# Kernel tuning notes

Hardware: AMD Instinct MI355X
Metric: run time of the kernel (lower is better)

Reference implementation:

```python
import jax, jax.numpy as jnp
import numpy as np

N_NODES = 100000
N_EDGES = 1600000
D_IN, D_HID, N_CLASSES = 128, 128, 64


def setup_inputs() -> dict:
    key = jax.random.key(0)
    k1, k2, k3, k4 = jax.random.split(key, 4)
    x = jax.random.normal(k1, (N_NODES, D_IN), dtype=jnp.float32)
    edge_index = jax.random.randint(k2, (2, N_EDGES), 0, N_NODES, dtype=jnp.int64)
    W1 = jax.random.normal(k3, (D_IN, D_HID), dtype=jnp.float32) * 0.05
    b1 = jnp.zeros((D_HID,), dtype=jnp.float32)
    W2 = jax.random.normal(k4, (D_HID, N_CLASSES), dtype=jnp.float32) * 0.05
    b2 = jnp.zeros((N_CLASSES,), dtype=jnp.float32)
    return {"x": x, "edge_index": edge_index, "W1": W1, "b1": b1, "W2": W2, "b2": b2}


def _gcn_layer(x, src_all, dst_all, edge_w, W, b):
    # PyG GCNConv: x' = D^{-1/2} (A + I) D^{-1/2} (x W) + b
    n = x.shape[0]
    h = x @ W                                   # [N, out]
    msg = h[src_all] * edge_w[:, None]          # [E+N, out]
    out = jax.ops.segment_sum(msg, dst_all, num_segments=n)
    return out + b


def reference(x, edge_index, W1, b1, W2, b2):
    n = x.shape[0]
    src, dst = edge_index[0], edge_index[1]
    loop = jnp.arange(n, dtype=src.dtype)
    src_all = jnp.concatenate([src, loop])      # self-loops added (GCNConv default)
    dst_all = jnp.concatenate([dst, loop])
    deg = jax.ops.segment_sum(jnp.ones_like(dst_all, dtype=x.dtype), dst_all,
                              num_segments=n)
    dinv = jnp.where(deg > 0, jax.lax.rsqrt(deg), 0.0)
    edge_w = dinv[src_all] * dinv[dst_all]      # symmetric normalization

    h = _gcn_layer(x, src_all, dst_all, edge_w, W1, b1)
    h = jax.nn.relu(h)                          # dropout is identity in eval mode
    h = _gcn_layer(h, src_all, dst_all, edge_w, W2, b2)
    return jax.nn.log_softmax(h, axis=1)
```

## Files before the change

### kernel.cpp

```cpp
#include <hip/hip_runtime.h>
#include <math.h>

#define DIN 128
#define NCLS 64
#define BSH  7
#define BSZ  128
#define BCAP 2816
#define SCALE1 64.0f
#define SCALE2 256.0f

typedef __attribute__((ext_vector_type(4))) float  f32x4;
typedef __attribute__((ext_vector_type(2))) float  f32x2;
typedef __attribute__((ext_vector_type(8))) short  bf16x8;

__device__ inline unsigned short f2bf(float f) {
    unsigned int u = __float_as_uint(f);
    u += 0x7fff + ((u >> 16) & 1);
    return (unsigned short)(u >> 16);
}


__global__ __launch_bounds__(256) void binA_k(const int* __restrict__ ei,
                                              int* __restrict__ gcnt,
                                              unsigned int* __restrict__ tmp,
                                              int E, int NB) {
    __shared__ int lcnt[1024];
    __shared__ int gpos[1024];
    const int t = threadIdx.x;
    for (int i = t; i < NB; i += 256) lcnt[i] = 0;
    __syncthreads();

    const int base = blockIdx.x * 4096;
    unsigned int pk[16];
    short bk[16], rk[16];
#pragma unroll
    for (int k = 0; k < 16; ++k) {
        int e = base + k * 256 + t;
        if (e < E) {
            int s = ei[e];
            int d = ei[E + e];
            int b = d >> BSH;
            pk[k] = ((unsigned int)s << BSH) | (unsigned int)(d & (BSZ - 1));
            bk[k] = (short)b;
            rk[k] = (short)atomicAdd(&lcnt[b], 1);
        } else {
            bk[k] = -1;
        }
    }
    __syncthreads();
    for (int i = t; i < NB; i += 256)
        gpos[i] = lcnt[i] ? atomicAdd(&gcnt[i], lcnt[i]) : 0;
    __syncthreads();
#pragma unroll
    for (int k = 0; k < 16; ++k) {
        if (bk[k] >= 0) {
            int b = bk[k];
            int pos = gpos[b] + rk[k];
            if (pos < BCAP) tmp[(size_t)b * BCAP + pos] = pk[k];
        }
    }
}

__global__ __launch_bounds__(1024) void scanb_k(const int* __restrict__ gcnt,
                                                int* __restrict__ bbase, int NB) {
    __shared__ int tmp[1024];
    int t = threadIdx.x;
    int v = (t < NB) ? gcnt[t] : 0;
    tmp[t] = v; __syncthreads();
    for (int o = 1; o < 1024; o <<= 1) {
        int x = (t >= o) ? tmp[t - o] : 0;
        __syncthreads();
        tmp[t] += x;
        __syncthreads();
    }
    if (t < NB) bbase[t] = (t == 0) ? 0 : tmp[t - 1];
}

__global__ __launch_bounds__(256) void binB_k(const unsigned int* __restrict__ tmp,
                                              const int* __restrict__ gcnt,
                                              const int* __restrict__ bbase,
                                              int* __restrict__ off,
                                              float* __restrict__ dinv,
                                              int* __restrict__ srcs,
                                              int N, int E) {
    __shared__ unsigned int stg[BCAP];
    __shared__ int lcnt[BSZ], sc[BSZ], loff[BSZ], lcur[BSZ];
    const int b = blockIdx.x, t = threadIdx.x;
    int cnt = gcnt[b];
    if (cnt > BCAP) cnt = BCAP;
    const int base = bbase[b];
    if (t < BSZ) { lcnt[t] = 0; lcur[t] = 0; }
    __syncthreads();
    for (int i = t; i < cnt; i += 256) {
        unsigned int v = tmp[(size_t)b * BCAP + i];
        stg[i] = v;
        atomicAdd(&lcnt[v & (BSZ - 1u)], 1);
    }
    __syncthreads();
    if (t < BSZ) sc[t] = lcnt[t];
    __syncthreads();
    for (int o = 1; o < BSZ; o <<= 1) {
        int x = 0;
        if (t < BSZ && t >= o) x = sc[t - o];
        __syncthreads();
        if (t < BSZ) sc[t] += x;
        __syncthreads();
    }
    if (t < BSZ) {
        int excl = (t == 0) ? 0 : sc[t - 1];
        loff[t] = excl;
        int node = b * BSZ + t;
        if (node <= N) off[node] = base + excl;
        if (node < N)  dinv[node] = rsqrtf(1.0f + (float)lcnt[t]);
    }
    __syncthreads();
    for (int i = t; i < cnt; i += 256) {
        unsigned int v = stg[i];
        int l = v & (BSZ - 1u);
        int r = atomicAdd(&lcur[l], 1);
        srcs[base + loff[l] + r] = (int)(v >> BSH);
    }
}


__global__ void wprep_k(const float* __restrict__ W1, const float* __restrict__ W2,
                        unsigned short* __restrict__ wt1, unsigned short* __restrict__ wt2,
                        int* __restrict__ gcnt, int NB) {
    int i = blockIdx.x * 256 + threadIdx.x;
    if (i < 128 * 128) { int k = i >> 7, n = i & 127; wt1[n * 128 + k] = f2bf(W1[i]); }
    if (i < 128 * 64)  { int k = i >> 6, n = i & 63;  wt2[n * 128 + k] = f2bf(W2[i]); }
    if (i < NB)        gcnt[i] = 0;
}


__global__ __launch_bounds__(256) void mgemm_k(const float* __restrict__ A,
                                               const unsigned short* __restrict__ Bt,
                                               const float* __restrict__ dinv,
                                               unsigned char* __restrict__ C,
                                               float oscale, int N) {
    constexpr int LDK = DIN + 8;
    constexpr int BN  = 128;
    __shared__ unsigned short As[64 * LDK];
    __shared__ unsigned short Bs[BN * LDK];
    const int tid  = threadIdx.x;
    const int row0 = blockIdx.x * 64;

    for (int idx = tid; idx < BN * 16; idx += 256) {
        int n = idx >> 4, c = (idx & 15) << 3;
        *(uint4*)&Bs[n * LDK + c] = *(const uint4*)&Bt[n * DIN + c];
    }
    for (int idx = tid; idx < 64 * 16; idx += 256) {
        int r = idx >> 4, c = (idx & 15) << 3;
        int gr = row0 + r;
        unsigned short v[8];
        if (gr < N) {
            f32x4 a0 = *(const f32x4*)&A[(size_t)gr * DIN + c];
            f32x4 a1 = *(const f32x4*)&A[(size_t)gr * DIN + c + 4];
            v[0] = f2bf(a0.x); v[1] = f2bf(a0.y); v[2] = f2bf(a0.z); v[3] = f2bf(a0.w);
            v[4] = f2bf(a1.x); v[5] = f2bf(a1.y); v[6] = f2bf(a1.z); v[7] = f2bf(a1.w);
        } else {
#pragma unroll
            for (int j = 0; j < 8; ++j) v[j] = 0;
        }
        *(uint4*)&As[r * LDK + c] = *(const uint4*)v;
    }
    __syncthreads();

    const int wave = tid >> 6, lane = tid & 63;
    const int lrow = lane & 15, kq = lane >> 4;
    constexpr int NT = BN / 16;
    f32x4 acc[NT];
#pragma unroll
    for (int t = 0; t < NT; ++t) acc[t] = (f32x4){0.f, 0.f, 0.f, 0.f};

    const unsigned short* Abase = &As[(wave * 16 + lrow) * LDK + kq * 8];
    const unsigned short* Bbase = &Bs[lrow * LDK + kq * 8];
#pragma unroll
    for (int kk = 0; kk < 4; ++kk) {
        bf16x8 a = *(const bf16x8*)(Abase + kk * 32);
#pragma unroll
        for (int t = 0; t < NT; ++t) {
            bf16x8 b = *(const bf16x8*)(Bbase + t * 16 * LDK + kk * 32);
            acc[t] = __builtin_amdgcn_mfma_f32_16x16x32_bf16(a, b, acc[t], 0, 0, 0);
        }
    }

    const int rb = row0 + wave * 16 + kq * 4;
#pragma unroll
    for (int r = 0; r < 4; ++r) {
        int gr = rb + r;
        if (gr < N) {
            float sc2 = dinv[gr] * oscale;
#pragma unroll
            for (int t = 0; t < NT; t += 2) {
                int pk = __builtin_amdgcn_cvt_pk_fp8_f32(acc[t][r] * sc2,
                                                         acc[t + 1][r] * sc2, 0, false);
                C[(size_t)gr * BN + t * 16 + lrow]       = (unsigned char)(pk & 0xff);
                C[(size_t)gr * BN + (t + 1) * 16 + lrow] = (unsigned char)((pk >> 8) & 0xff);
            }
        }
    }
}

__device__ inline void dec8(uint2 v, f32x2& x0, f32x2& x1, f32x2& x2, f32x2& x3) {
    x0 += __builtin_amdgcn_cvt_pk_f32_fp8((int)v.x, false);
    x1 += __builtin_amdgcn_cvt_pk_f32_fp8((int)v.x, true);
    x2 += __builtin_amdgcn_cvt_pk_f32_fp8((int)v.y, false);
    x3 += __builtin_amdgcn_cvt_pk_f32_fp8((int)v.y, true);
}

__device__ inline void dec16(uint4 v, f32x2& x0, f32x2& x1, f32x2& x2, f32x2& x3,
                             f32x2& x4, f32x2& x5, f32x2& x6, f32x2& x7) {
    x0 += __builtin_amdgcn_cvt_pk_f32_fp8((int)v.x, false);
    x1 += __builtin_amdgcn_cvt_pk_f32_fp8((int)v.x, true);
    x2 += __builtin_amdgcn_cvt_pk_f32_fp8((int)v.y, false);
    x3 += __builtin_amdgcn_cvt_pk_f32_fp8((int)v.y, true);
    x4 += __builtin_amdgcn_cvt_pk_f32_fp8((int)v.z, false);
    x5 += __builtin_amdgcn_cvt_pk_f32_fp8((int)v.z, true);
    x6 += __builtin_amdgcn_cvt_pk_f32_fp8((int)v.w, false);
    x7 += __builtin_amdgcn_cvt_pk_f32_fp8((int)v.w, true);
}


__global__ __launch_bounds__(512, 8) void fuse2_k(const unsigned char* __restrict__ hs,
                                                  const int* __restrict__ off,
                                                  const int* __restrict__ srcs,
                                                  const float* __restrict__ dinv,
                                                  const float* __restrict__ b1,
                                                  const unsigned short* __restrict__ Bt,
                                                  unsigned char* __restrict__ C,
                                                  int N) {
    constexpr int LDK = DIN + 8;
    __shared__ unsigned short As[64 * LDK];
    __shared__ unsigned short Bs[NCLS * LDK];
    const int tid  = threadIdx.x;
    const int row0 = blockIdx.x * 64;

    for (int idx = tid; idx < NCLS * 16; idx += 512) {
        int n = idx >> 4, c = (idx & 15) << 3;
        *(uint4*)&Bs[n * LDK + c] = *(const uint4*)&Bt[n * DIN + c];
    }

    const int oc = tid >> 3;
    const int sl = tid & 7;
    const int node = row0 + oc;
    const uint4* hp = (const uint4*)hs;

    if (node < N) {
        const int beg = off[node], end = off[node + 1];
        f32x2 a0={0.f,0.f},a1={0.f,0.f},a2={0.f,0.f},a3={0.f,0.f};
        f32x2 a4={0.f,0.f},a5={0.f,0.f},a6={0.f,0.f},a7={0.f,0.f};
        int i = beg;
        for (; i + 3 < end; i += 4) {
            unsigned s0 = (unsigned)srcs[i],     s1 = (unsigned)srcs[i + 1];
            unsigned s2 = (unsigned)srcs[i + 2], s3 = (unsigned)srcs[i + 3];
            uint4 v0 = hp[s0 * 8u + sl];
            uint4 v1 = hp[s1 * 8u + sl];
            uint4 v2 = hp[s2 * 8u + sl];
            uint4 v3 = hp[s3 * 8u + sl];
            dec16(v0, a0,a1,a2,a3,a4,a5,a6,a7);
            dec16(v1, a0,a1,a2,a3,a4,a5,a6,a7);
            dec16(v2, a0,a1,a2,a3,a4,a5,a6,a7);
            dec16(v3, a0,a1,a2,a3,a4,a5,a6,a7);
        }
        for (; i < end; ++i) {
            uint4 v = hp[(unsigned)srcs[i] * 8u + sl];
            dec16(v, a0,a1,a2,a3,a4,a5,a6,a7);
        }
        {
            uint4 v = hp[(unsigned)node * 8u + sl];
            dec16(v, a0,a1,a2,a3,a4,a5,a6,a7);
        }
        const float d = dinv[node] * (1.0f / SCALE1);
        const float4 w0 = ((const float4*)b1)[sl * 4 + 0];
        const float4 w1 = ((const float4*)b1)[sl * 4 + 1];
        const float4 w2 = ((const float4*)b1)[sl * 4 + 2];
        const float4 w3 = ((const float4*)b1)[sl * 4 + 3];
        float o0  = fmaxf(fmaf(d, a0.x, w0.x), 0.f);
        float o1  = fmaxf(fmaf(d, a0.y, w0.y), 0.f);
        float o2  = fmaxf(fmaf(d, a1.x, w0.z), 0.f);
        float o3  = fmaxf(fmaf(d, a1.y, w0.w), 0.f);
        float o4  = fmaxf(fmaf(d, a2.x, w1.x), 0.f);
        float o5  = fmaxf(fmaf(d, a2.y, w1.y), 0.f);
        float o6  = fmaxf(fmaf(d, a3.x, w1.z), 0.f);
        float o7  = fmaxf(fmaf(d, a3.y, w1.w), 0.f);
        float o8  = fmaxf(fmaf(d, a4.x, w2.x), 0.f);
        float o9  = fmaxf(fmaf(d, a4.y, w2.y), 0.f);
        float o10 = fmaxf(fmaf(d, a5.x, w2.z), 0.f);
        float o11 = fmaxf(fmaf(d, a5.y, w2.w), 0.f);
        float o12 = fmaxf(fmaf(d, a6.x, w3.x), 0.f);
        float o13 = fmaxf(fmaf(d, a6.y, w3.y), 0.f);
        float o14 = fmaxf(fmaf(d, a7.x, w3.z), 0.f);
        float o15 = fmaxf(fmaf(d, a7.y, w3.w), 0.f);
        uint4 u0, u1;
        u0.x = (unsigned)f2bf(o0)  | ((unsigned)f2bf(o1)  << 16);
        u0.y = (unsigned)f2bf(o2)  | ((unsigned)f2bf(o3)  << 16);
        u0.z = (unsigned)f2bf(o4)  | ((unsigned)f2bf(o5)  << 16);
        u0.w = (unsigned)f2bf(o6)  | ((unsigned)f2bf(o7)  << 16);
        u1.x = (unsigned)f2bf(o8)  | ((unsigned)f2bf(o9)  << 16);
        u1.y = (unsigned)f2bf(o10) | ((unsigned)f2bf(o11) << 16);
        u1.z = (unsigned)f2bf(o12) | ((unsigned)f2bf(o13) << 16);
        u1.w = (unsigned)f2bf(o14) | ((unsigned)f2bf(o15) << 16);
        *(uint4*)&As[oc * LDK + sl * 16]     = u0;
        *(uint4*)&As[oc * LDK + sl * 16 + 8] = u1;
    } else {
        uint4 z = make_uint4(0, 0, 0, 0);
        *(uint4*)&As[oc * LDK + sl * 16]     = z;
        *(uint4*)&As[oc * LDK + sl * 16 + 8] = z;
    }
    __syncthreads();

    const int wave = tid >> 6, lane = tid & 63;
    const int ws = wave & 3;
    const int ch = wave >> 2;
    const int lrow = lane & 15, kq = lane >> 4;
    f32x4 acc0 = (f32x4){0.f,0.f,0.f,0.f};
    f32x4 acc1 = (f32x4){0.f,0.f,0.f,0.f};

    const unsigned short* Abase = &As[(ws * 16 + lrow) * LDK + kq * 8];
    const unsigned short* Bbase = &Bs[(ch * 32 + lrow) * LDK + kq * 8];
#pragma unroll
    for (int kk = 0; kk < 4; ++kk) {
        bf16x8 a  = *(const bf16x8*)(Abase + kk * 32);
        bf16x8 b0 = *(const bf16x8*)(Bbase + kk * 32);
        bf16x8 b1v= *(const bf16x8*)(Bbase + 16 * LDK + kk * 32);
        acc0 = __builtin_amdgcn_mfma_f32_16x16x32_bf16(a, b0,  acc0, 0, 0, 0);
        acc1 = __builtin_amdgcn_mfma_f32_16x16x32_bf16(a, b1v, acc1, 0, 0, 0);
    }

    const int rb = row0 + ws * 16 + kq * 4;
#pragma unroll
    for (int r = 0; r < 4; ++r) {
        int gr = rb + r;
        if (gr < N) {
            float sc2 = dinv[gr] * SCALE2;
            int pk = __builtin_amdgcn_cvt_pk_fp8_f32(acc0[r] * sc2, acc1[r] * sc2, 0, false);
            C[(size_t)gr * NCLS + ch * 32 + lrow]      = (unsigned char)(pk & 0xff);
            C[(size_t)gr * NCLS + ch * 32 + 16 + lrow] = (unsigned char)((pk >> 8) & 0xff);
        }
    }
}


__global__ __launch_bounds__(256) void gather2_k(const unsigned char* __restrict__ hs,
                                                 const int* __restrict__ off,
                                                 const int* __restrict__ srcs,
                                                 const float* __restrict__ dinv,
                                                 const float* __restrict__ b2,
                                                 float* __restrict__ out, int N) {
    const int lane = threadIdx.x & 63;
    const int wave = threadIdx.x >> 6;
    const int o8 = lane >> 3;
    const int sl = lane & 7;
    const int node = blockIdx.x * 32 + wave * 8 + o8;
    if (node >= N) return;
    const int beg = off[node], end = off[node + 1];
    const uint2* hp = (const uint2*)hs;
    f32x2 A0 = {0.f,0.f}, A1 = {0.f,0.f}, A2 = {0.f,0.f}, A3 = {0.f,0.f};
    f32x2 C0 = {0.f,0.f}, C1 = {0.f,0.f}, C2 = {0.f,0.f}, C3 = {0.f,0.f};
    int i = beg;
    for (; i + 7 < end; i += 8) {
        unsigned s0 = (unsigned)srcs[i],     s1 = (unsigned)srcs[i + 1];
        unsigned s2 = (unsigned)srcs[i + 2], s3 = (unsigned)srcs[i + 3];
        unsigned s4 = (unsigned)srcs[i + 4], s5 = (unsigned)srcs[i + 5];
        unsigned s6 = (unsigned)srcs[i + 6], s7 = (unsigned)srcs[i + 7];
        uint2 v0 = hp[s0 * 8u + sl];
        uint2 v1 = hp[s1 * 8u + sl];
        uint2 v2 = hp[s2 * 8u + sl];
        uint2 v3 = hp[s3 * 8u + sl];
        uint2 v4 = hp[s4 * 8u + sl];
        uint2 v5 = hp[s5 * 8u + sl];
        uint2 v6 = hp[s6 * 8u + sl];
        uint2 v7 = hp[s7 * 8u + sl];
        dec8(v0, A0, A1, A2, A3);
        dec8(v1, C0, C1, C2, C3);
        dec8(v2, A0, A1, A2, A3);
        dec8(v3, C0, C1, C2, C3);
        dec8(v4, A0, A1, A2, A3);
        dec8(v5, C0, C1, C2, C3);
        dec8(v6, A0, A1, A2, A3);
        dec8(v7, C0, C1, C2, C3);
    }
    for (; i + 3 < end; i += 4) {
        unsigned s0 = (unsigned)srcs[i],     s1 = (unsigned)srcs[i + 1];
        unsigned s2 = (unsigned)srcs[i + 2], s3 = (unsigned)srcs[i + 3];
        uint2 v0 = hp[s0 * 8u + sl];
        uint2 v1 = hp[s1 * 8u + sl];
        uint2 v2 = hp[s2 * 8u + sl];
        uint2 v3 = hp[s3 * 8u + sl];
        dec8(v0, A0, A1, A2, A3);
        dec8(v1, C0, C1, C2, C3);
        dec8(v2, A0, A1, A2, A3);
        dec8(v3, C0, C1, C2, C3);
    }
    for (; i < end; ++i) {
        uint2 v = hp[(unsigned)srcs[i] * 8u + sl];
        dec8(v, A0, A1, A2, A3);
    }
    {
        uint2 v = hp[(unsigned)node * 8u + sl];
        dec8(v, C0, C1, C2, C3);
    }
    A0 += C0; A1 += C1; A2 += C2; A3 += C3;

    float d = dinv[node] * (1.0f / SCALE2);
    float4 ba = ((const float4*)b2)[sl * 2];
    float4 bb = ((const float4*)b2)[sl * 2 + 1];
    float v0 = fmaf(d, A0.x, ba.x);
    float v1 = fmaf(d, A0.y, ba.y);
    float v2 = fmaf(d, A1.x, ba.z);
    float v3 = fmaf(d, A1.y, ba.w);
    float v4 = fmaf(d, A2.x, bb.x);
    float v5 = fmaf(d, A2.y, bb.y);
    float v6 = fmaf(d, A3.x, bb.z);
    float v7 = fmaf(d, A3.y, bb.w);
    float m = fmaxf(fmaxf(fmaxf(v0, v1), fmaxf(v2, v3)), fmaxf(fmaxf(v4, v5), fmaxf(v6, v7)));
#pragma unroll
    for (int mk = 1; mk <= 4; mk <<= 1) m = fmaxf(m, __shfl_xor(m, mk, 64));
    float s = __expf(v0 - m) + __expf(v1 - m) + __expf(v2 - m) + __expf(v3 - m)
            + __expf(v4 - m) + __expf(v5 - m) + __expf(v6 - m) + __expf(v7 - m);
#pragma unroll
    for (int mk = 1; mk <= 4; mk <<= 1) s += __shfl_xor(s, mk, 64);
    float ls = m + __logf(s);
    float4 oa, ob;
    oa.x = v0 - ls; oa.y = v1 - ls; oa.z = v2 - ls; oa.w = v3 - ls;
    ob.x = v4 - ls; ob.y = v5 - ls; ob.z = v6 - ls; ob.w = v7 - ls;
    ((float4*)out)[(unsigned)node * 16u + sl * 2]     = oa;
    ((float4*)out)[(unsigned)node * 16u + sl * 2 + 1] = ob;
}


extern "C" void kernel_launch(void* const* d_in, const int* in_sizes, int n_in,
                              void* d_out, int out_size, void* d_ws, size_t ws_size,
                              hipStream_t stream) {
    const float* x  = (const float*)d_in[0];
    const int*   ei = (const int*)d_in[1];
    const float* W1 = (const float*)d_in[2];
    const float* b1 = (const float*)d_in[3];
    const float* W2 = (const float*)d_in[4];
    const float* b2 = (const float*)d_in[5];
    float* out = (float*)d_out;

    const int N  = in_sizes[0] / DIN;
    const int E  = in_sizes[1] / 2;
    const int NB = (N + BSZ - 1) >> BSH;

    char* p = (char*)d_ws;
    auto alloc = [&](size_t bytes) { void* r = p; p += (bytes + 255) & ~(size_t)255; return r; };
    float* dinv  = (float*)alloc((size_t)N * 4);
    int*   gcnt  = (int*)  alloc((size_t)NB * 4);
    int*   bbase = (int*)  alloc((size_t)NB * 4);
    int*   off   = (int*)  alloc((size_t)(N + 1) * 4);
    int*   srcs  = (int*)  alloc((size_t)E * 4);
    unsigned int* tmp = (unsigned int*)alloc((size_t)NB * BCAP * 4);
    unsigned short* wt1 = (unsigned short*)alloc(128 * 128 * 2);
    unsigned short* wt2 = (unsigned short*)alloc(64 * 128 * 2);
    unsigned char*  hs1 = (unsigned char*)alloc((size_t)N * DIN);
    unsigned char*  hs2 = (unsigned char*)alloc((size_t)N * NCLS);

    wprep_k<<<64, 256, 0, stream>>>(W1, W2, wt1, wt2, gcnt, NB);
    binA_k<<<(E + 4095) / 4096, 256, 0, stream>>>(ei, gcnt, tmp, E, NB);
    scanb_k<<<1, 1024, 0, stream>>>(gcnt, bbase, NB);
    binB_k<<<NB, 256, 0, stream>>>(tmp, gcnt, bbase, off, dinv, srcs, N, E);

    mgemm_k<<<(N + 63) / 64, 256, 0, stream>>>(x, wt1, dinv, hs1, SCALE1, N);
    fuse2_k<<<(N + 63) / 64, 512, 0, stream>>>(hs1, off, srcs, dinv, b1, wt2, hs2, N);
    gather2_k<<<(N + 31) / 32, 256, 0, stream>>>(hs2, off, srcs, dinv, b2, out, N);
}
```

Measured before the change: 213.3 us.

## Compute degrees with global atomics and merge CSR build with first GEMM launch

Node degrees are now counted with global atomics during binning, so the first GEMM no longer waits on the per-bucket CSR build to get dinv. The CSR build and the first feature GEMM run as one launch that splits blocks by index, letting the two independent tasks overlap and dropping one kernel launch. Each consumer recomputes rsqrt from the integer degree instead of reading a precomputed dinv. In exchange, binA issues 1.6M global atomics, wprep now launches enough blocks to zero the degree array, and bmix's shared-memory footprint is the larger of the two uses.

```diff
diff --git a/kernel.cpp b/kernel.cpp
--- a/kernel.cpp
+++ b/kernel.cpp
@@ -20,8 +20,23 @@
 }
 
 
+__global__ __launch_bounds__(256) void wprep_k(const float* __restrict__ W1,
+                                               const float* __restrict__ W2,
+                                               unsigned short* __restrict__ wt1,
+                                               unsigned short* __restrict__ wt2,
+                                               int* __restrict__ deg,
+                                               int* __restrict__ gcnt, int N, int NB) {
+    int i = blockIdx.x * 256 + threadIdx.x;
+    if (i < 128 * 128) { int k = i >> 7, n = i & 127; wt1[n * 128 + k] = f2bf(W1[i]); }
+    if (i < 128 * 64)  { int k = i >> 6, n = i & 63;  wt2[n * 128 + k] = f2bf(W2[i]); }
+    if (i < N)         deg[i] = 0;
+    if (i < NB)        gcnt[i] = 0;
+}
+
+
 __global__ __launch_bounds__(256) void binA_k(const int* __restrict__ ei,
                                               int* __restrict__ gcnt,
+                                              int* __restrict__ deg,
                                               unsigned int* __restrict__ tmp,
                                               int E, int NB) {
     __shared__ int lcnt[1024];
@@ -39,6 +54,7 @@
         if (e < E) {
             int s = ei[e];
             int d = ei[E + e];
+            atomicAdd(&deg[d], 1);
             int b = d >> BSH;
             pk[k] = ((unsigned int)s << BSH) | (unsigned int)(d & (BSZ - 1));
             bk[k] = (short)b;
@@ -76,80 +92,75 @@
     if (t < NB) bbase[t] = (t == 0) ? 0 : tmp[t - 1];
 }
 
-__global__ __launch_bounds__(256) void binB_k(const unsigned int* __restrict__ tmp,
+
+__global__ __launch_bounds__(256) void bmix_k(const unsigned int* __restrict__ tmp,
                                               const int* __restrict__ gcnt,
                                               const int* __restrict__ bbase,
                                               int* __restrict__ off,
-                                              float* __restrict__ dinv,
                                               int* __restrict__ srcs,
-                                              int N, int E) {
-    __shared__ unsigned int stg[BCAP];
-    __shared__ int lcnt[BSZ], sc[BSZ], loff[BSZ], lcur[BSZ];
-    const int b = blockIdx.x, t = threadIdx.x;
-    int cnt = gcnt[b];
-    if (cnt > BCAP) cnt = BCAP;
-    const int base = bbase[b];
-    if (t < BSZ) { lcnt[t] = 0; lcur[t] = 0; }
-    __syncthreads();
-    for (int i = t; i < cnt; i += 256) {
-        unsigned int v = tmp[(size_t)b * BCAP + i];
-        stg[i] = v;
-        atomicAdd(&lcnt[v & (BSZ - 1u)], 1);
-    }
-    __syncthreads();
-    if (t < BSZ) sc[t] = lcnt[t];
-    __syncthreads();
-    for (int o = 1; o < BSZ; o <<= 1) {
-        int x = 0;
-        if (t < BSZ && t >= o) x = sc[t - o];
-        __syncthreads();
-        if (t < BSZ) sc[t] += x;
-        __syncthreads();
-    }
-    if (t < BSZ) {
-        int excl = (t == 0) ? 0 : sc[t - 1];
-        loff[t] = excl;
-        int node = b * BSZ + t;
-        if (node <= N) off[node] = base + excl;
-        if (node < N)  dinv[node] = rsqrtf(1.0f + (float)lcnt[t]);
-    }
-    __syncthreads();
-    for (int i = t; i < cnt; i += 256) {
-        unsigned int v = stg[i];
-        int l = v & (BSZ - 1u);
-        int r = atomicAdd(&lcur[l], 1);
-        srcs[base + loff[l] + r] = (int)(v >> BSH);
-    }
-}
-
-
-__global__ void wprep_k(const float* __restrict__ W1, const float* __restrict__ W2,
-                        unsigned short* __restrict__ wt1, unsigned short* __restrict__ wt2,
-                        int* __restrict__ gcnt, int NB) {
-    int i = blockIdx.x * 256 + threadIdx.x;
-    if (i < 128 * 128) { int k = i >> 7, n = i & 127; wt1[n * 128 + k] = f2bf(W1[i]); }
-    if (i < 128 * 64)  { int k = i >> 6, n = i & 63;  wt2[n * 128 + k] = f2bf(W2[i]); }
-    if (i < NB)        gcnt[i] = 0;
-}
-
-
-__global__ __launch_bounds__(256) void mgemm_k(const float* __restrict__ A,
-                                               const unsigned short* __restrict__ Bt,
-                                               const float* __restrict__ dinv,
-                                               unsigned char* __restrict__ C,
-                                               float oscale, int N) {
+                                              int N, int E, int NB,
+                                              const float* __restrict__ A,
+                                              const unsigned short* __restrict__ Bt,
+                                              const int* __restrict__ deg,
+                                              unsigned char* __restrict__ C,
+                                              float oscale) {
     constexpr int LDK = DIN + 8;
     constexpr int BN  = 128;
-    __shared__ unsigned short As[64 * LDK];
-    __shared__ unsigned short Bs[BN * LDK];
-    const int tid  = threadIdx.x;
-    const int row0 = blockIdx.x * 64;
-
-    for (int idx = tid; idx < BN * 16; idx += 256) {
+    __shared__ __align__(16) unsigned char raw[64 * LDK * 2 + BN * LDK * 2];
+    const int t = threadIdx.x;
+
+    if ((int)blockIdx.x < NB) {
+        unsigned int* stg  = (unsigned int*)raw;
+        int* lcnt = (int*)(raw + BCAP * 4);
+        int* sc   = lcnt + BSZ;
+        int* loff = sc + BSZ;
+        int* lcur = loff + BSZ;
+        const int b = blockIdx.x;
+        int cnt = gcnt[b];
+        if (cnt > BCAP) cnt = BCAP;
+        const int base = bbase[b];
+        if (t < BSZ) { lcnt[t] = 0; lcur[t] = 0; }
+        __syncthreads();
+        for (int i = t; i < cnt; i += 256) {
+            unsigned int v = tmp[(size_t)b * BCAP + i];
+            stg[i] = v;
+            atomicAdd(&lcnt[v & (BSZ - 1u)], 1);
+        }
+        __syncthreads();
+        if (t < BSZ) sc[t] = lcnt[t];
+        __syncthreads();
+        for (int o = 1; o < BSZ; o <<= 1) {
+            int x = 0;
+            if (t < BSZ && t >= o) x = sc[t - o];
+            __syncthreads();
+            if (t < BSZ) sc[t] += x;
+            __syncthreads();
+        }
+        if (t < BSZ) {
+            int excl = (t == 0) ? 0 : sc[t - 1];
+            loff[t] = excl;
+            int node = b * BSZ + t;
+            if (node <= N) off[node] = base + excl;
+        }
+        __syncthreads();
+        for (int i = t; i < cnt; i += 256) {
+            unsigned int v = stg[i];
+            int l = v & (BSZ - 1u);
+            int r = atomicAdd(&lcur[l], 1);
+            srcs[base + loff[l] + r] = (int)(v >> BSH);
+        }
+        return;
+    }
+
+    unsigned short* As = (unsigned short*)raw;
+    unsigned short* Bs = As + 64 * LDK;
+    const int row0 = ((int)blockIdx.x - NB) * 64;
+
+    for (int idx = t; idx < BN * 16; idx += 256) {
         int n = idx >> 4, c = (idx & 15) << 3;
         *(uint4*)&Bs[n * LDK + c] = *(const uint4*)&Bt[n * DIN + c];
     }
-    for (int idx = tid; idx < 64 * 16; idx += 256) {
+    for (int idx = t; idx < 64 * 16; idx += 256) {
         int r = idx >> 4, c = (idx & 15) << 3;
         int gr = row0 + r;
         unsigned short v[8];
@@ -166,12 +177,12 @@
     }
     __syncthreads();
 
-    const int wave = tid >> 6, lane = tid & 63;
+    const int wave = t >> 6, lane = t & 63;
     const int lrow = lane & 15, kq = lane >> 4;
     constexpr int NT = BN / 16;
     f32x4 acc[NT];
 #pragma unroll
-    for (int t = 0; t < NT; ++t) acc[t] = (f32x4){0.f, 0.f, 0.f, 0.f};
+    for (int q = 0; q < NT; ++q) acc[q] = (f32x4){0.f, 0.f, 0.f, 0.f};
 
     const unsigned short* Abase = &As[(wave * 16 + lrow) * LDK + kq * 8];
     const unsigned short* Bbase = &Bs[lrow * LDK + kq * 8];
@@ -179,9 +190,9 @@
     for (int kk = 0; kk < 4; ++kk) {
         bf16x8 a = *(const bf16x8*)(Abase + kk * 32);
 #pragma unroll
-        for (int t = 0; t < NT; ++t) {
-            bf16x8 b = *(const bf16x8*)(Bbase + t * 16 * LDK + kk * 32);
-            acc[t] = __builtin_amdgcn_mfma_f32_16x16x32_bf16(a, b, acc[t], 0, 0, 0);
+        for (int q = 0; q < NT; ++q) {
+            bf16x8 b = *(const bf16x8*)(Bbase + q * 16 * LDK + kk * 32);
+            acc[q] = __builtin_amdgcn_mfma_f32_16x16x32_bf16(a, b, acc[q], 0, 0, 0);
         }
     }
 
@@ -190,13 +201,13 @@
     for (int r = 0; r < 4; ++r) {
         int gr = rb + r;
         if (gr < N) {
-            float sc2 = dinv[gr] * oscale;
-#pragma unroll
-            for (int t = 0; t < NT; t += 2) {
-                int pk = __builtin_amdgcn_cvt_pk_fp8_f32(acc[t][r] * sc2,
-                                                         acc[t + 1][r] * sc2, 0, false);
-                C[(size_t)gr * BN + t * 16 + lrow]       = (unsigned char)(pk & 0xff);
-                C[(size_t)gr * BN + (t + 1) * 16 + lrow] = (unsigned char)((pk >> 8) & 0xff);
+            float sc2 = rsqrtf(1.0f + (float)deg[gr]) * oscale;
+#pragma unroll
+            for (int q = 0; q < NT; q += 2) {
+                int pk = __builtin_amdgcn_cvt_pk_fp8_f32(acc[q][r] * sc2,
+                                                         acc[q + 1][r] * sc2, 0, false);
+                C[(size_t)gr * BN + q * 16 + lrow]       = (unsigned char)(pk & 0xff);
+                C[(size_t)gr * BN + (q + 1) * 16 + lrow] = (unsigned char)((pk >> 8) & 0xff);
             }
         }
     }
@@ -225,7 +236,7 @@
 __global__ __launch_bounds__(512, 8) void fuse2_k(const unsigned char* __restrict__ hs,
                                                   const int* __restrict__ off,
                                                   const int* __restrict__ srcs,
-                                                  const float* __restrict__ dinv,
+                                                  const int* __restrict__ deg,
                                                   const float* __restrict__ b1,
                                                   const unsigned short* __restrict__ Bt,
                                                   unsigned char* __restrict__ C,
@@ -271,7 +282,7 @@
             uint4 v = hp[(unsigned)node * 8u + sl];
             dec16(v, a0,a1,a2,a3,a4,a5,a6,a7);
         }
-        const float d = dinv[node] * (1.0f / SCALE1);
+        const float d = rsqrtf(1.0f + (float)deg[node]) * (1.0f / SCALE1);
         const float4 w0 = ((const float4*)b1)[sl * 4 + 0];
         const float4 w1 = ((const float4*)b1)[sl * 4 + 1];
         const float4 w2 = ((const float4*)b1)[sl * 4 + 2];
@@ -333,7 +344,7 @@
     for (int r = 0; r < 4; ++r) {
         int gr = rb + r;
         if (gr < N) {
-            float sc2 = dinv[gr] * SCALE2;
+            float sc2 = rsqrtf(1.0f + (float)deg[gr]) * SCALE2;
             int pk = __builtin_amdgcn_cvt_pk_fp8_f32(acc0[r] * sc2, acc1[r] * sc2, 0, false);
             C[(size_t)gr * NCLS + ch * 32 + lrow]      = (unsigned char)(pk & 0xff);
             C[(size_t)gr * NCLS + ch * 32 + 16 + lrow] = (unsigned char)((pk >> 8) & 0xff);
@@ -345,7 +356,7 @@
 __global__ __launch_bounds__(256) void gather2_k(const unsigned char* __restrict__ hs,
                                                  const int* __restrict__ off,
                                                  const int* __restrict__ srcs,
-                                                 const float* __restrict__ dinv,
+                                                 const int* __restrict__ deg,
                                                  const float* __restrict__ b2,
                                                  float* __restrict__ out, int N) {
     const int lane = threadIdx.x & 63;
@@ -403,7 +414,7 @@
     }
     A0 += C0; A1 += C1; A2 += C2; A3 += C3;
 
-    float d = dinv[node] * (1.0f / SCALE2);
+    float d = rsqrtf(1.0f + (float)deg[node]) * (1.0f / SCALE2);
     float4 ba = ((const float4*)b2)[sl * 2];
     float4 bb = ((const float4*)b2)[sl * 2 + 1];
     float v0 = fmaf(d, A0.x, ba.x);
@@ -444,10 +455,11 @@
     const int N  = in_sizes[0] / DIN;
     const int E  = in_sizes[1] / 2;
     const int NB = (N + BSZ - 1) >> BSH;
+    const int NG = (N + 63) / 64;
 
     char* p = (char*)d_ws;
     auto alloc = [&](size_t bytes) { void* r = p; p += (bytes + 255) & ~(size_t)255; return r; };
-    float* dinv  = (float*)alloc((size_t)N * 4);
+    int*   deg   = (int*)  alloc((size_t)N * 4);
     int*   gcnt  = (int*)  alloc((size_t)NB * 4);
     int*   bbase = (int*)  alloc((size_t)NB * 4);
     int*   off   = (int*)  alloc((size_t)(N + 1) * 4);
@@ -458,12 +470,11 @@
     unsigned char*  hs1 = (unsigned char*)alloc((size_t)N * DIN);
     unsigned char*  hs2 = (unsigned char*)alloc((size_t)N * NCLS);
 
-    wprep_k<<<64, 256, 0, stream>>>(W1, W2, wt1, wt2, gcnt, NB);
-    binA_k<<<(E + 4095) / 4096, 256, 0, stream>>>(ei, gcnt, tmp, E, NB);
+    wprep_k<<<(N + 255) / 256, 256, 0, stream>>>(W1, W2, wt1, wt2, deg, gcnt, N, NB);
+    binA_k<<<(E + 4095) / 4096, 256, 0, stream>>>(ei, gcnt, deg, tmp, E, NB);
     scanb_k<<<1, 1024, 0, stream>>>(gcnt, bbase, NB);
-    binB_k<<<NB, 256, 0, stream>>>(tmp, gcnt, bbase, off, dinv, srcs, N, E);
-
-    mgemm_k<<<(N + 63) / 64, 256, 0, stream>>>(x, wt1, dinv, hs1, SCALE1, N);
-    fuse2_k<<<(N + 63) / 64, 512, 0, stream>>>(hs1, off, srcs, dinv, b1, wt2, hs2, N);
-    gather2_k<<<(N + 31) / 32, 256, 0, stream>>>(hs2, off, srcs, dinv, b2, out, N);
-}
+    bmix_k<<<NB + NG, 256, 0, stream>>>(tmp, gcnt, bbase, off, srcs, N, E, NB,
+                                        x, wt1, deg, hs1, SCALE1);
+    fuse2_k<<<(N + 63) / 64, 512, 0, stream>>>(hs1, off, srcs, deg, b1, wt2, hs2, N);
+    gather2_k<<<(N + 31) / 32, 256, 0, stream>>>(hs2, off, srcs, deg, b2, out, N);
+}
```

New measurement: 267.6 us. 25.4% more time.
